# Kernel optimization log

Measured on AMD Instinct MI355X. Metric: run time of the kernel, lower is better.

The kernel has to match this reference:

```python
import jax, jax.numpy as jnp
import numpy as np

N = 400000  # active sparse points (voxels)
K = 27      # 3^3 kernel offsets (dimension=3, kernel_size=3)
C = 32      # inplanes == planes
EPS = 1e-5


def sparse_conv(x, nbr, mask, W, b):
    # gather-GEMM-scatter: for each kernel offset k, out += x[nbr[:,k]] @ W[k]
    # missing neighbors are masked out (MinkowskiEngine skips absent pairs).
    xg = x[nbr] * mask[..., None].astype(x.dtype)   # [N, K, C]
    return jnp.einsum('nkc,kcd->nd', xg, W) + b     # [N, C]


def batchnorm(h, gamma, beta):
    # MinkowskiBatchNorm: per-channel stats over all active points
    mean = jnp.mean(h, axis=0)
    var = jnp.mean(jnp.square(h - mean), axis=0)
    return (h - mean) * jax.lax.rsqrt(var + EPS) * gamma + beta


def setup_inputs() -> dict:
    key = jax.random.key(0)
    ks = jax.random.split(key, 13)
    x = jax.random.normal(ks[0], (N, C), dtype=jnp.float32)
    nbr1 = jax.random.randint(ks[1], (N, K), 0, N, dtype=jnp.int32)
    mask1 = jax.random.randint(ks[2], (N, K), 0, 2, dtype=jnp.int32).astype(bool)
    nbr2 = jax.random.randint(ks[3], (N, K), 0, N, dtype=jnp.int32)
    mask2 = jax.random.randint(ks[4], (N, K), 0, 2, dtype=jnp.int32).astype(bool)
    s = 1.0 / np.sqrt(K * C)  # kaiming-ish scale for sparse conv kernels
    W1 = jax.random.normal(ks[5], (K, C, C), dtype=jnp.float32) * s
    b1 = jax.random.normal(ks[6], (C,), dtype=jnp.float32) * 0.01
    W2 = jax.random.normal(ks[7], (K, C, C), dtype=jnp.float32) * s
    b2 = jax.random.normal(ks[8], (C,), dtype=jnp.float32) * 0.01
    gamma1 = jnp.ones((C,), jnp.float32)
    beta1 = jnp.zeros((C,), jnp.float32)
    gamma2 = jnp.ones((C,), jnp.float32)
    beta2 = jnp.zeros((C,), jnp.float32)
    return dict(x=x, W1=W1, b1=b1, gamma1=gamma1, beta1=beta1,
                W2=W2, b2=b2, gamma2=gamma2, beta2=beta2,
                nbr1=nbr1, mask1=mask1, nbr2=nbr2, mask2=mask2)


def reference(x, W1, b1, gamma1, beta1, W2, b2, gamma2, beta2,
              nbr1, mask1, nbr2, mask2):
    residual = x  # downsample = Identity (stride=1)
    out = sparse_conv(x, nbr1, mask1, W1, b1)
    out = jax.nn.relu(batchnorm(out, gamma1, beta1))
    out = sparse_conv(out, nbr2, mask2, W2, b2)
    out = batchnorm(out, gamma2, beta2)
    out = out + residual  # drop_path=0.0 -> Identity
    return jax.nn.relu(out)
```

## Files before the change

kernel.cpp:

```cpp
#include <hip/hip_runtime.h>

#define NPTS 400000
#define KK 27
#define CC 32
#define EPSV 1e-5f
#define LSTRIDE 29

using bf8_t = __attribute__((ext_vector_type(8))) __bf16;
using f4_t  = __attribute__((ext_vector_type(4))) float;
using us8_t = __attribute__((ext_vector_type(8))) unsigned short;

__device__ __forceinline__ unsigned short f2bf(float f) {
    unsigned int u = __float_as_uint(f);
    u += 0x7FFF + ((u >> 16) & 1u);
    return (unsigned short)(u >> 16);
}

#define WBLOCKS 216
__global__ __launch_bounds__(256) void cvt_all(
    const float* __restrict__ x,
    const float* __restrict__ W1, const float* __restrict__ W2,
    unsigned short* __restrict__ xb,
    unsigned short* __restrict__ Wt1, unsigned short* __restrict__ Wt2)
{
    const int bid = blockIdx.x;
    if (bid < WBLOCKS) {
        const int id = bid * 256 + threadIdx.x;
        const int which = id >= KK * CC * CC;
        const int t = which ? id - KK * CC * CC : id;
        const int k = t >> 10, d = (t >> 5) & 31, c = t & 31;
        const float* W = which ? W2 : W1;
        unsigned short* Wt = which ? Wt2 : Wt1;
        Wt[t] = f2bf(W[k * 1024 + c * CC + d]);
        return;
    }
    const size_t base = ((size_t)(bid - WBLOCKS) * 256 + threadIdx.x) * 8;
    if (base >= (size_t)NPTS * CC) return;
    const f4_t v0 = *(const f4_t*)(x + base);
    const f4_t v1 = *(const f4_t*)(x + base + 4);
    us8_t o;
#pragma unroll
    for (int j = 0; j < 8; ++j) o[j] = f2bf(j < 4 ? v0[j] : v1[j - 4]);
    *(us8_t*)(xb + base) = o;
}

__global__ __launch_bounds__(256, 4) void conv_mfma(
    const unsigned short* __restrict__ xb,
    const unsigned short* __restrict__ Wt,
    const float* __restrict__ bias,
    const int* __restrict__ nbr,
    const int* __restrict__ mask,
    float* __restrict__ out,
    float* __restrict__ sums)
{
    __shared__ int lidx[128 * LSTRIDE];
    __shared__ float rs[4][CC], rq[4][CC];

    const int t = threadIdx.x;
    const int P0 = blockIdx.x * 128;

    const int* nb = nbr + (size_t)P0 * KK;
    const int* mb = mask + (size_t)P0 * KK;
    for (int i = t; i < 128 * KK; i += 256) {
        const int p = i / KK;
        const int k = i - p * KK;
        lidx[p * LSTRIDE + k] = mb[i] ? nb[i] : -1;
    }
    __syncthreads();

    const int wave = t >> 6;
    const int lane = t & 63;
    const int m = lane & 15;
    const int q = lane >> 4;
    const int p0 = P0 + wave * 32;

    const int* rowA = lidx + (wave * 32 + m) * LSTRIDE;
    const int* rowB = rowA + 16 * LSTRIDE;

    f4_t acc00 = {}, acc01 = {}, acc10 = {}, acc11 = {};

#pragma unroll
    for (int kb = 0; kb < 3; ++kb) {
        bf8_t A0[9], A1[9];
#pragma unroll
        for (int j = 0; j < 9; ++j) {
            const int i0 = rowA[kb * 9 + j];
            const int i1 = rowB[kb * 9 + j];
            bf8_t t0 = {}, t1 = {};
            if (i0 >= 0) t0 = *(const bf8_t*)(xb + i0 * CC + q * 8);
            if (i1 >= 0) t1 = *(const bf8_t*)(xb + i1 * CC + q * 8);
            A0[j] = t0; A1[j] = t1;
        }
#pragma unroll
        for (int j = 0; j < 9; ++j) {
            const unsigned short* wk = Wt + (kb * 9 + j) * (CC * CC) + q * 8;
            const bf8_t w0 = *(const bf8_t*)(wk + m * CC);
            const bf8_t w1 = *(const bf8_t*)(wk + (m + 16) * CC);
            acc00 = __builtin_amdgcn_mfma_f32_16x16x32_bf16(A0[j], w0, acc00, 0, 0, 0);
            acc01 = __builtin_amdgcn_mfma_f32_16x16x32_bf16(A0[j], w1, acc01, 0, 0, 0);
            acc10 = __builtin_amdgcn_mfma_f32_16x16x32_bf16(A1[j], w0, acc10, 0, 0, 0);
            acc11 = __builtin_amdgcn_mfma_f32_16x16x32_bf16(A1[j], w1, acc11, 0, 0, 0);
        }
    }

    const float b0 = bias[m], b1 = bias[m + 16];
    float s0 = 0.f, q0 = 0.f, s1 = 0.f, q1 = 0.f;
#pragma unroll
    for (int g = 0; g < 2; ++g) {
        const f4_t t0v = g ? acc10 : acc00;
        const f4_t t1v = g ? acc11 : acc01;
        const int prow = p0 + 16 * g + q * 4;
#pragma unroll
        for (int r = 0; r < 4; ++r) {
            const float v0 = t0v[r] + b0;
            const float v1 = t1v[r] + b1;
            out[(size_t)(prow + r) * CC + m] = v0;
            out[(size_t)(prow + r) * CC + m + 16] = v1;
            s0 += v0; q0 += v0 * v0;
            s1 += v1; q1 += v1 * v1;
        }
    }
    s0 += __shfl_down(s0, 32, 64); s0 += __shfl_down(s0, 16, 64);
    q0 += __shfl_down(q0, 32, 64); q0 += __shfl_down(q0, 16, 64);
    s1 += __shfl_down(s1, 32, 64); s1 += __shfl_down(s1, 16, 64);
    q1 += __shfl_down(q1, 32, 64); q1 += __shfl_down(q1, 16, 64);

    if (lane < 16) {
        rs[wave][m] = s0;      rq[wave][m] = q0;
        rs[wave][m + 16] = s1; rq[wave][m + 16] = q1;
    }
    __syncthreads();
    if (t < CC) {
        atomicAdd(&sums[t],      rs[0][t] + rs[1][t] + rs[2][t] + rs[3][t]);
        atomicAdd(&sums[CC + t], rq[0][t] + rq[1][t] + rq[2][t] + rq[3][t]);
    }
}

__global__ __launch_bounds__(256) void bn_relu_bf16(
    const float* __restrict__ h, const float* __restrict__ sums,
    const float* __restrict__ gamma, const float* __restrict__ beta,
    unsigned short* __restrict__ buf)
{
    const size_t base = ((size_t)blockIdx.x * 256 + threadIdx.x) * 8;
    if (base >= (size_t)NPTS * CC) return;
    const int d0 = (int)(base & (CC - 1));
    const f4_t v0 = *(const f4_t*)(h + base);
    const f4_t v1 = *(const f4_t*)(h + base + 4);
    us8_t o;
#pragma unroll
    for (int j = 0; j < 8; ++j) {
        const int d = d0 + j;
        const float mean = sums[d] * (1.f / NPTS);
        const float var = sums[CC + d] * (1.f / NPTS) - mean * mean;
        const float sc = gamma[d] * rsqrtf(var + EPSV);
        const float x = (j < 4 ? v0[j] : v1[j - 4]);
        o[j] = f2bf(fmaxf((x - mean) * sc + beta[d], 0.f));
    }
    *(us8_t*)(buf + base) = o;
}

__global__ __launch_bounds__(256) void bn_res_relu_kernel(
    float* __restrict__ out, const float* __restrict__ sums,
    const float* __restrict__ gamma, const float* __restrict__ beta,
    const float* __restrict__ x)
{
    const size_t i = (size_t)blockIdx.x * 256 + threadIdx.x;
    const size_t base = i * 4;
    if (base >= (size_t)NPTS * CC) return;
    const int d0 = (int)(base & (CC - 1));
    float4 v = ((const float4*)out)[i];
    float4 rx = ((const float4*)x)[i];
    float r[4] = {v.x, v.y, v.z, v.w};
    const float rxf[4] = {rx.x, rx.y, rx.z, rx.w};
#pragma unroll
    for (int j = 0; j < 4; ++j) {
        const int d = d0 + j;
        const float mean = sums[d] * (1.f / NPTS);
        const float var = sums[CC + d] * (1.f / NPTS) - mean * mean;
        const float sc = gamma[d] * rsqrtf(var + EPSV);
        r[j] = fmaxf((r[j] - mean) * sc + beta[d] + rxf[j], 0.f);
    }
    ((float4*)out)[i] = make_float4(r[0], r[1], r[2], r[3]);
}

extern "C" void kernel_launch(void* const* d_in, const int* in_sizes, int n_in,
                              void* d_out, int out_size, void* d_ws, size_t ws_size,
                              hipStream_t stream) {
    const float* x   = (const float*)d_in[0];
    const float* W1  = (const float*)d_in[1];
    const float* b1  = (const float*)d_in[2];
    const float* g1  = (const float*)d_in[3];
    const float* be1 = (const float*)d_in[4];
    const float* W2  = (const float*)d_in[5];
    const float* b2  = (const float*)d_in[6];
    const float* g2  = (const float*)d_in[7];
    const float* be2 = (const float*)d_in[8];
    const int* nbr1  = (const int*)d_in[9];
    const int* mask1 = (const int*)d_in[10];
    const int* nbr2  = (const int*)d_in[11];
    const int* mask2 = (const int*)d_in[12];

    float* out = (float*)d_out;

    float* sums          = (float*)d_ws;
    unsigned short* xbuf = (unsigned short*)((char*)d_ws + 1024);
    unsigned short* Wt1  = xbuf + (size_t)NPTS * CC;
    unsigned short* Wt2  = Wt1 + KK * CC * CC;

    hipMemsetAsync(d_ws, 0, 1024, stream);

    const int cvt_blocks = WBLOCKS + (NPTS * CC / 8 + 255) / 256;

    cvt_all<<<cvt_blocks, 256, 0, stream>>>(x, W1, W2, xbuf, Wt1, Wt2);
    conv_mfma<<<NPTS / 128, 256, 0, stream>>>(xbuf, Wt1, b1, nbr1, mask1, out, sums);
    bn_relu_bf16<<<(NPTS * CC / 8 + 255) / 256, 256, 0, stream>>>(out, sums, g1, be1, xbuf);
    conv_mfma<<<NPTS / 128, 256, 0, stream>>>(xbuf, Wt2, b2, nbr2, mask2, out, sums + 64);
    bn_res_relu_kernel<<<(NPTS * CC / 4 + 255) / 256, 256, 0, stream>>>(out, sums + 64, g2, be2, x);
}
```

Measured before the change: 538.8 us.

## Software-pipeline neighbor gathers with zero row and padded kernel offsets

Masked-out neighbors now point to an extra all-zero row at index NPTS, which removes the per-load branch. The kernel offsets are padded from 27 to 28 with zero weights, so the gather-MFMA loop runs as four chunks of seven. The next chunk's gathers are issued before the current chunk's MFMAs, using double-buffered registers and sched_barrier. Occupancy hint drops from 4 to 3 blocks per CU to make room for the extra live registers, and the padding adds one wasted offset of work per point.

```diff
diff --git a/kernel.cpp b/kernel.cpp
--- a/kernel.cpp
+++ b/kernel.cpp
@@ -2,6 +2,7 @@
 
 #define NPTS 400000
 #define KK 27
+#define KP 28
 #define CC 32
 #define EPSV 1e-5f
 #define LSTRIDE 29
@@ -16,7 +17,7 @@
     return (unsigned short)(u >> 16);
 }
 
-#define WBLOCKS 216
+#define WBLOCKS 224
 __global__ __launch_bounds__(256) void cvt_all(
     const float* __restrict__ x,
     const float* __restrict__ W1, const float* __restrict__ W2,
@@ -26,16 +27,21 @@
     const int bid = blockIdx.x;
     if (bid < WBLOCKS) {
         const int id = bid * 256 + threadIdx.x;
-        const int which = id >= KK * CC * CC;
-        const int t = which ? id - KK * CC * CC : id;
+        const int which = id >= KP * CC * CC;
+        const int t = which ? id - KP * CC * CC : id;
         const int k = t >> 10, d = (t >> 5) & 31, c = t & 31;
         const float* W = which ? W2 : W1;
         unsigned short* Wt = which ? Wt2 : Wt1;
-        Wt[t] = f2bf(W[k * 1024 + c * CC + d]);
+        Wt[t] = (k < KK) ? f2bf(W[k * 1024 + c * CC + d]) : (unsigned short)0;
         return;
     }
     const size_t base = ((size_t)(bid - WBLOCKS) * 256 + threadIdx.x) * 8;
-    if (base >= (size_t)NPTS * CC) return;
+    if (base >= (size_t)(NPTS + 1) * CC) return;
+    if (base >= (size_t)NPTS * CC) {
+        us8_t z = {};
+        *(us8_t*)(xb + base) = z;
+        return;
+    }
     const f4_t v0 = *(const f4_t*)(x + base);
     const f4_t v1 = *(const f4_t*)(x + base + 4);
     us8_t o;
@@ -44,7 +50,7 @@
     *(us8_t*)(xb + base) = o;
 }
 
-__global__ __launch_bounds__(256, 4) void conv_mfma(
+__global__ __launch_bounds__(256, 3) void conv_mfma(
     const unsigned short* __restrict__ xb,
     const unsigned short* __restrict__ Wt,
     const float* __restrict__ bias,
@@ -64,8 +70,9 @@
     for (int i = t; i < 128 * KK; i += 256) {
         const int p = i / KK;
         const int k = i - p * KK;
-        lidx[p * LSTRIDE + k] = mb[i] ? nb[i] : -1;
-    }
+        lidx[p * LSTRIDE + k] = mb[i] ? nb[i] : NPTS;
+    }
+    if (t < 128) lidx[t * LSTRIDE + KK] = NPTS;
     __syncthreads();
 
     const int wave = t >> 6;
@@ -78,28 +85,38 @@
     const int* rowB = rowA + 16 * LSTRIDE;
 
     f4_t acc00 = {}, acc01 = {}, acc10 = {}, acc11 = {};
-
-#pragma unroll
-    for (int kb = 0; kb < 3; ++kb) {
-        bf8_t A0[9], A1[9];
-#pragma unroll
-        for (int j = 0; j < 9; ++j) {
-            const int i0 = rowA[kb * 9 + j];
-            const int i1 = rowB[kb * 9 + j];
-            bf8_t t0 = {}, t1 = {};
-            if (i0 >= 0) t0 = *(const bf8_t*)(xb + i0 * CC + q * 8);
-            if (i1 >= 0) t1 = *(const bf8_t*)(xb + i1 * CC + q * 8);
-            A0[j] = t0; A1[j] = t1;
-        }
-#pragma unroll
-        for (int j = 0; j < 9; ++j) {
-            const unsigned short* wk = Wt + (kb * 9 + j) * (CC * CC) + q * 8;
+    bf8_t A0[7], A1[7], B0[7], B1[7];
+
+#pragma unroll
+    for (int j = 0; j < 7; ++j) {
+        A0[j] = *(const bf8_t*)(xb + rowA[j] * CC + q * 8);
+        A1[j] = *(const bf8_t*)(xb + rowB[j] * CC + q * 8);
+    }
+
+#pragma unroll
+    for (int kb = 0; kb < 4; ++kb) {
+        if (kb < 3) {
+#pragma unroll
+            for (int j = 0; j < 7; ++j) {
+                B0[j] = *(const bf8_t*)(xb + rowA[(kb + 1) * 7 + j] * CC + q * 8);
+                B1[j] = *(const bf8_t*)(xb + rowB[(kb + 1) * 7 + j] * CC + q * 8);
+            }
+        }
+        __builtin_amdgcn_sched_barrier(0);
+#pragma unroll
+        for (int j = 0; j < 7; ++j) {
+            const unsigned short* wk = Wt + (kb * 7 + j) * (CC * CC) + q * 8;
             const bf8_t w0 = *(const bf8_t*)(wk + m * CC);
             const bf8_t w1 = *(const bf8_t*)(wk + (m + 16) * CC);
             acc00 = __builtin_amdgcn_mfma_f32_16x16x32_bf16(A0[j], w0, acc00, 0, 0, 0);
             acc01 = __builtin_amdgcn_mfma_f32_16x16x32_bf16(A0[j], w1, acc01, 0, 0, 0);
             acc10 = __builtin_amdgcn_mfma_f32_16x16x32_bf16(A1[j], w0, acc10, 0, 0, 0);
             acc11 = __builtin_amdgcn_mfma_f32_16x16x32_bf16(A1[j], w1, acc11, 0, 0, 0);
+        }
+        __builtin_amdgcn_sched_barrier(0);
+        if (kb < 3) {
+#pragma unroll
+            for (int j = 0; j < 7; ++j) { A0[j] = B0[j]; A1[j] = B1[j]; }
         }
     }
 
@@ -204,12 +221,12 @@
 
     float* sums          = (float*)d_ws;
     unsigned short* xbuf = (unsigned short*)((char*)d_ws + 1024);
-    unsigned short* Wt1  = xbuf + (size_t)NPTS * CC;
-    unsigned short* Wt2  = Wt1 + KK * CC * CC;
+    unsigned short* Wt1  = xbuf + (size_t)(NPTS + 1) * CC;
+    unsigned short* Wt2  = Wt1 + KP * CC * CC;
 
     hipMemsetAsync(d_ws, 0, 1024, stream);
 
-    const int cvt_blocks = WBLOCKS + (NPTS * CC / 8 + 255) / 256;
+    const int cvt_blocks = WBLOCKS + (int)(((size_t)(NPTS + 1) * CC / 8 + 255) / 256);
 
     cvt_all<<<cvt_blocks, 256, 0, stream>>>(x, W1, W2, xbuf, Wt1, Wt2);
     conv_mfma<<<NPTS / 128, 256, 0, stream>>>(xbuf, Wt1, b1, nbr1, mask1, out, sums);
```

New measurement: 584.0 us. +8.4%, slower.
